# Performance work log

Hardware: AMD Instinct MI355X
Metric: run time of the kernel (lower is better)

Reference implementation:

```python
import jax, jax.numpy as jnp
import numpy as np

B, Q, C, H, N, D, F = 1, 2048, 2048, 1024, 16, 64, 4096
R = Q + C  # relative position encoding length
EPS = 1e-12
NEG = 1e30


def setup_inputs() -> dict:
    key = jax.random.key(0)
    ks = jax.random.split(key, 16)
    s = 0.02
    return dict(
        content_stream=jax.random.normal(ks[0], (B, Q, H), jnp.float32),
        content_mask=jnp.zeros((B, 1, Q, C), jnp.float32),
        context=jax.random.normal(ks[1], (B, C, H), jnp.float32),
        position_encoding=jax.random.normal(ks[2], (B, R, H), jnp.float32),
        content_bias=jax.random.normal(ks[3], (N, D), jnp.float32) * s,
        position_bias=jax.random.normal(ks[4], (N, D), jnp.float32) * s,
        segment_encoding=jax.random.normal(ks[5], (2, N, D), jnp.float32) * s,
        segment_matrix=jax.random.randint(ks[6], (B, Q, C), 0, 2).astype(bool),
        segment_bias=jax.random.normal(ks[7], (N, D), jnp.float32) * s,
        Wq=jax.random.normal(ks[8], (H, N, D), jnp.float32) * s,
        Wk=jax.random.normal(ks[9], (H, N, D), jnp.float32) * s,
        Wv=jax.random.normal(ks[10], (H, N, D), jnp.float32) * s,
        Wr=jax.random.normal(ks[11], (H, N, D), jnp.float32) * s,
        Wo=jax.random.normal(ks[12], (H, N, D), jnp.float32) * s,
        ln1_gamma=jnp.ones((H,), jnp.float32),
        ln1_beta=jnp.zeros((H,), jnp.float32),
        W1=jax.random.normal(ks[13], (H, F), jnp.float32) * s,
        b1=jnp.zeros((F,), jnp.float32),
        W2=jax.random.normal(ks[14], (F, H), jnp.float32) * s,
        b2=jnp.zeros((H,), jnp.float32),
        ln2_gamma=jnp.ones((H,), jnp.float32),
        ln2_beta=jnp.zeros((H,), jnp.float32),
    )


def _layernorm(x, g, b):
    m = jnp.mean(x, axis=-1, keepdims=True)
    v = jnp.mean(jnp.square(x - m), axis=-1, keepdims=True)
    return (x - m) * jax.lax.rsqrt(v + EPS) * g + b


def _rel_shift(x, klen):
    # x: [b, n, q, r] -> shifted [b, n, q, klen] (XLNet reshape trick)
    b, n, q, r = x.shape
    x = x.reshape(b, n, r, q)[:, :, 1:, :].reshape(b, n, q, r - 1)
    return x[:, :, :, :klen]


def reference(content_stream, content_mask, context, position_encoding,
              content_bias, position_bias, segment_encoding, segment_matrix,
              segment_bias, Wq, Wk, Wv, Wr, Wo, ln1_gamma, ln1_beta,
              W1, b1, W2, b2, ln2_gamma, ln2_beta):
    q = jnp.einsum('bqh,hnd->bqnd', content_stream, Wq)
    k = jnp.einsum('bch,hnd->bcnd', context, Wk)
    v = jnp.einsum('bch,hnd->bcnd', context, Wv)
    r = jnp.einsum('brh,hnd->brnd', position_encoding, Wr)

    # content / position / segment bias terms (XLNet relative attention)
    ac = jnp.einsum('bqnd,bcnd->bnqc', q + content_bias, k)
    bd = _rel_shift(jnp.einsum('bqnd,brnd->bnqr', q + position_bias, r),
                    k.shape[1])
    ef = jnp.einsum('bqnd,snd->bnqs', q + segment_bias, segment_encoding)
    ef = jnp.where(segment_matrix[:, None], ef[..., 1:], ef[..., :1])

    scores = (ac + bd + ef) / jnp.sqrt(jnp.float32(D))
    scores = scores - NEG * content_mask  # mask: 1.0 = disallowed
    probs = jax.nn.softmax(scores, axis=-1)

    attn = jnp.einsum('bnqc,bcnd->bqnd', probs, v)
    attn_out = jnp.einsum('bqnd,hnd->bqh', attn, Wo)

    # residual + LN, then FFN, residual + LN (dropout off: training=False)
    ffn_in = _layernorm(attn_out + content_stream, ln1_gamma, ln1_beta)
    ffn_out = jax.nn.relu(ffn_in @ W1 + b1) @ W2 + b2
    return _layernorm(ffn_out + ffn_in, ln2_gamma, ln2_beta)
```

## Files before the change

### kernel.cpp

```cpp
#include <hip/hip_runtime.h>
#include <stdint.h>


typedef unsigned short ushort_t;
typedef __attribute__((ext_vector_type(8))) short bf16x8;
typedef __attribute__((ext_vector_type(4))) float f32x4;

#define QLEN 2048
#define CLEN 2048
#define HDIM 1024
#define NHEAD 16
#define DHEAD 64
#define RLEN 4096
#define FDIM 4096

__device__ __forceinline__ float bf2f(ushort_t u) {
  union { float f; uint32_t i; } x; x.i = ((uint32_t)u) << 16; return x.f;
}
__device__ __forceinline__ ushort_t f2bf(float f) {
  union { float f; uint32_t i; } x; x.f = f;
  uint32_t r = x.i + 0x7fffu + ((x.i >> 16) & 1u);
  return (ushort_t)(r >> 16);
}
__device__ __forceinline__ f32x4 mfma16(bf16x8 a, bf16x8 b, f32x4 c) {
  return __builtin_amdgcn_mfma_f32_16x16x32_bf16(a, b, c, 0, 0, 0);
}
__device__ __forceinline__ bool probe_bf16(const uint32_t* probe) {
  return probe[0] == 0x3F803F80u;
}

typedef const __attribute__((address_space(1))) void* gas_t;
typedef __attribute__((address_space(3))) void* las_t;
__device__ __forceinline__ void glds16(const void* g, void* l) {
  __builtin_amdgcn_global_load_lds((gas_t)(uintptr_t)g, (las_t)(uintptr_t)l, 16, 0, 0);
}

__device__ __forceinline__ void bar_lds() {
  __asm__ volatile("s_waitcnt lgkmcnt(0)\n\ts_barrier" ::: "memory");
}
__device__ __forceinline__ void bar_full() {
  __asm__ volatile("s_waitcnt vmcnt(0) lgkmcnt(0)\n\ts_barrier" ::: "memory");
}

struct ConvJobs {
  const void* src[5];
  const void* mask_src;
  ushort_t* dst[5];
  int n[5];
  int blk0[6];
};

__global__ __launch_bounds__(256) void conv_all(
    ConvJobs J, const uint32_t* __restrict__ probe)
{
  const bool isb = probe_bf16(probe);
  int j = 0;
  #pragma unroll
  for (int t = 1; t < 5; t++) if ((int)blockIdx.x >= J.blk0[t]) j = t;
  const int lb = blockIdx.x - J.blk0[j];
  const int nb = J.blk0[j + 1] - J.blk0[j];
  const int n = J.n[j];
  ushort_t* dst = J.dst[j];
  if (j < 4) {
    const void* src = J.src[j];
    for (int i = lb * 256 + threadIdx.x; i < n; i += nb * 256)
      dst[i] = isb ? ((const ushort_t*)src)[i] : f2bf(((const float*)src)[i]);
  } else {
    const void* sm = J.src[4];
    uint32_t sw = 0;
    #pragma unroll
    for (int t = 0; t < 8; t++) sw |= ((const uint32_t*)sm)[t];
    const bool i8 = sw > 1u;
    for (int i = lb * 256 + threadIdx.x; i < n; i += nb * 256) {
      const int s = i8 ? (int)((const unsigned char*)sm)[i]
                       : (int)((const uint32_t*)sm)[i];
      const float mv = isb ? bf2f(((const ushort_t*)J.mask_src)[i])
                           : ((const float*)J.mask_src)[i];
      const float f = (float)(s ? 1 : 0) + (mv != 0.f ? 2.f : 0.f);
      dst[i] = f2bf(f);
    }
  }
}

struct SmallBatch {
  const void* src[10];
  int n[10];
  int off[10];
};

__global__ __launch_bounds__(256) void convert_small(
    SmallBatch sb, ushort_t* __restrict__ dst, const uint32_t* __restrict__ probe)
{
  const bool isb = probe_bf16(probe);
  const int t = blockIdx.x;
  const void* s = sb.src[t];
  ushort_t* d = dst + sb.off[t];
  for (int i = threadIdx.x; i < sb.n[t]; i += 256)
    d[i] = isb ? ((const ushort_t*)s)[i] : f2bf(((const float*)s)[i]);
}

struct TransJobs { const void* src[4]; ushort_t* dst[4]; };
__global__ __launch_bounds__(256) void transpose4_to_bf16(
    TransJobs T, int R, int C, const uint32_t* __restrict__ probe)
{
  const bool isb = probe_bf16(probe);
  const void* in = T.src[blockIdx.z];
  ushort_t* out = T.dst[blockIdx.z];
  __shared__ ushort_t t[32][33];
  const int bx = blockIdx.x * 32, by = blockIdx.y * 32;
  const int x = threadIdx.x & 31, y0 = threadIdx.x >> 5;
  #pragma unroll
  for (int yy = 0; yy < 32; yy += 8) {
    const size_t idx = (size_t)(by + y0 + yy) * C + bx + x;
    t[y0 + yy][x] = isb ? ((const ushort_t*)in)[idx] : f2bf(((const float*)in)[idx]);
  }
  __syncthreads();
  #pragma unroll
  for (int yy = 0; yy < 32; yy += 8)
    out[(size_t)(bx + y0 + yy) * R + by + x] = t[x][y0 + yy];
}

__global__ __launch_bounds__(256) void transpose_to_bf16(
    const void* __restrict__ in, ushort_t* __restrict__ out, int R, int C,
    const uint32_t* __restrict__ probe)
{
  const bool isb = probe_bf16(probe);
  __shared__ ushort_t t[32][33];
  const int bx = blockIdx.x * 32, by = blockIdx.y * 32;
  const int x = threadIdx.x & 31, y0 = threadIdx.x >> 5;
  #pragma unroll
  for (int yy = 0; yy < 32; yy += 8) {
    const size_t idx = (size_t)(by + y0 + yy) * C + bx + x;
    t[y0 + yy][x] = isb ? ((const ushort_t*)in)[idx] : f2bf(((const float*)in)[idx]);
  }
  __syncthreads();
  #pragma unroll
  for (int yy = 0; yy < 32; yy += 8)
    out[(size_t)(bx + y0 + yy) * R + by + x] = t[x][y0 + yy];
}

__device__ __forceinline__ void gemm_store(
    void* out, const ushort_t* bias, int M, int N, int epi,
    int gm, int gn, float v)
{
  if (epi == 0) {
    ((ushort_t*)out)[(size_t)gm * N + gn] = f2bf(v);
  } else if (epi == 1) {
    ((ushort_t*)out)[(size_t)gn * M + gm] = f2bf(v);
  } else if (epi == 2) {
    ((float*)out)[(size_t)gm * N + gn] = v;
  } else if (epi == 3) {
    v += bf2f(bias[gn]); v = v > 0.f ? v : 0.f;
    ((ushort_t*)out)[(size_t)gm * N + gn] = f2bf(v);
  } else if (epi == 4) {
    v += bf2f(bias[gn]);
    ((float*)out)[(size_t)gm * N + gn] = v;
  } else if (epi == 5) {
    ((ushort_t*)out)[((size_t)(gn >> 6) * M + gm) * 64 + (gn & 63)] = f2bf(v);
  } else {
    if (gn < 1024)
      ((ushort_t*)out)[((size_t)(gn >> 6) * M + gm) * 64 + (gn & 63)] = f2bf(v);
    else
      ((ushort_t*)out)[(size_t)2097152 + (size_t)(gn - 1024) * M + gm] = f2bf(v);
  }
}

__global__ __launch_bounds__(256) void gemm_bt_kernel(
    const ushort_t* __restrict__ A, const ushort_t* __restrict__ Bt,
    const ushort_t* __restrict__ bias, void* __restrict__ out,
    int M, int N, int K, int epi)
{
  __shared__ __attribute__((aligned(16))) ushort_t As[2][128 * 32];
  __shared__ __attribute__((aligned(16))) ushort_t Bs[2][64 * 32];
  const int tid = threadIdx.x;
  const int lane = tid & 63, wave = tid >> 6;
  const int l15 = lane & 15, quad = lane >> 4;
  const int m0 = blockIdx.y * 128, n0 = blockIdx.x * 64;

  const int arow = tid >> 2;
  const int acol = (tid & 3) * 8;

  f32x4 acc[2][4];
  #pragma unroll
  for (int i = 0; i < 2; i++)
    #pragma unroll
    for (int j = 0; j < 4; j++) acc[i][j] = (f32x4){0.f, 0.f, 0.f, 0.f};

  const int KI = K >> 5;
  glds16(&A[(size_t)(m0 + arow) * K + acol], &As[0][tid * 8]);
  glds16(&A[(size_t)(m0 + arow + 64) * K + acol], &As[0][tid * 8 + 2048]);
  glds16(&Bt[(size_t)(n0 + arow) * K + acol], &Bs[0][tid * 8]);
  bar_full();

  for (int ki = 0; ki < KI; ki++) {
    const int b = ki & 1;
    if (ki + 1 < KI) {
      const int k1 = (ki + 1) << 5;
      glds16(&A[(size_t)(m0 + arow) * K + k1 + acol], &As[b ^ 1][tid * 8]);
      glds16(&A[(size_t)(m0 + arow + 64) * K + k1 + acol], &As[b ^ 1][tid * 8 + 2048]);
      glds16(&Bt[(size_t)(n0 + arow) * K + k1 + acol], &Bs[b ^ 1][tid * 8]);
    }
    bf16x8 af[2], bfr[4];
    #pragma unroll
    for (int i = 0; i < 2; i++)
      af[i] = *(const bf16x8*)&As[b][(wave * 32 + i * 16 + l15) * 32 + quad * 8];
    #pragma unroll
    for (int j = 0; j < 4; j++)
      bfr[j] = *(const bf16x8*)&Bs[b][(j * 16 + l15) * 32 + quad * 8];
    #pragma unroll
    for (int i = 0; i < 2; i++)
      #pragma unroll
      for (int j = 0; j < 4; j++)
        acc[i][j] = mfma16(af[i], bfr[j], acc[i][j]);
    bar_full();
  }

  #pragma unroll
  for (int i = 0; i < 2; i++)
    #pragma unroll
    for (int j = 0; j < 4; j++)
      #pragma unroll
      for (int rg = 0; rg < 4; rg++)
        gemm_store(out, bias, M, N, epi,
                   m0 + wave * 32 + i * 16 + quad * 4 + rg,
                   n0 + j * 16 + l15, acc[i][j][rg]);
}

struct Ptr4 { void* p[4]; };
__global__ __launch_bounds__(256) void gemm128_bt_kernel(
    const ushort_t* __restrict__ A, const ushort_t* __restrict__ Bt,
    const ushort_t* __restrict__ bias, Ptr4 outs,
    int M, int N, int K, int Kc, int epi)
{
  __shared__ __attribute__((aligned(16))) ushort_t As[2][128 * 32];
  __shared__ __attribute__((aligned(16))) ushort_t Bs[2][128 * 32];
  const int tid = threadIdx.x;
  const int lane = tid & 63, wave = tid >> 6;
  const int l15 = lane & 15, quad = lane >> 4;
  const int wm = wave >> 1, wn = wave & 1;
  const int m0 = blockIdx.y * 128, n0 = blockIdx.x * 128;
  const int kb = blockIdx.z * Kc;
  void* out = outs.p[blockIdx.z];

  const int arow = tid >> 2;
  const int acol = (tid & 3) * 8;

  f32x4 acc[4][4];
  #pragma unroll
  for (int i = 0; i < 4; i++)
    #pragma unroll
    for (int j = 0; j < 4; j++) acc[i][j] = (f32x4){0.f, 0.f, 0.f, 0.f};

  const int KI = Kc >> 5;
  glds16(&A[(size_t)(m0 + arow) * K + kb + acol], &As[0][tid * 8]);
  glds16(&A[(size_t)(m0 + arow + 64) * K + kb + acol], &As[0][tid * 8 + 2048]);
  glds16(&Bt[(size_t)(n0 + arow) * K + kb + acol], &Bs[0][tid * 8]);
  glds16(&Bt[(size_t)(n0 + arow + 64) * K + kb + acol], &Bs[0][tid * 8 + 2048]);
  bar_full();

  for (int ki = 0; ki < KI; ki++) {
    const int b = ki & 1;
    if (ki + 1 < KI) {
      const int k1 = kb + ((ki + 1) << 5);
      glds16(&A[(size_t)(m0 + arow) * K + k1 + acol], &As[b ^ 1][tid * 8]);
      glds16(&A[(size_t)(m0 + arow + 64) * K + k1 + acol], &As[b ^ 1][tid * 8 + 2048]);
      glds16(&Bt[(size_t)(n0 + arow) * K + k1 + acol], &Bs[b ^ 1][tid * 8]);
      glds16(&Bt[(size_t)(n0 + arow + 64) * K + k1 + acol], &Bs[b ^ 1][tid * 8 + 2048]);
    }
    bf16x8 af[4], bfr[4];
    #pragma unroll
    for (int i = 0; i < 4; i++)
      af[i] = *(const bf16x8*)&As[b][(wm * 64 + i * 16 + l15) * 32 + quad * 8];
    #pragma unroll
    for (int j = 0; j < 4; j++)
      bfr[j] = *(const bf16x8*)&Bs[b][(wn * 64 + j * 16 + l15) * 32 + quad * 8];
    #pragma unroll
    for (int i = 0; i < 4; i++)
      #pragma unroll
      for (int j = 0; j < 4; j++)
        acc[i][j] = mfma16(af[i], bfr[j], acc[i][j]);
    bar_full();
  }

  #pragma unroll
  for (int i = 0; i < 4; i++)
    #pragma unroll
    for (int j = 0; j < 4; j++)
      #pragma unroll
      for (int rg = 0; rg < 4; rg++)
        gemm_store(out, bias, M, N, epi,
                   m0 + wm * 64 + i * 16 + quad * 4 + rg,
                   n0 + wn * 64 + j * 16 + l15, acc[i][j][rg]);
}

__global__ __launch_bounds__(256) void gemm64_bt_kernel(
    const ushort_t* __restrict__ A, const ushort_t* __restrict__ Bt,
    const ushort_t* __restrict__ bias, void* __restrict__ out,
    int M, int N, int K, int epi)
{
  __shared__ __attribute__((aligned(16))) ushort_t As[2][64 * 32];
  __shared__ __attribute__((aligned(16))) ushort_t Bs[2][64 * 32];
  const int tid = threadIdx.x;
  const int lane = tid & 63, wave = tid >> 6;
  const int l15 = lane & 15, quad = lane >> 4;
  const int wm = wave >> 1, wn = wave & 1;
  const int m0 = blockIdx.y * 64, n0 = blockIdx.x * 64;

  const int arow = tid >> 2;
  const int acol = (tid & 3) * 8;

  f32x4 acc[2][2];
  #pragma unroll
  for (int i = 0; i < 2; i++)
    #pragma unroll
    for (int j = 0; j < 2; j++) acc[i][j] = (f32x4){0.f, 0.f, 0.f, 0.f};

  const int KI = K >> 5;
  glds16(&A[(size_t)(m0 + arow) * K + acol], &As[0][tid * 8]);
  glds16(&Bt[(size_t)(n0 + arow) * K + acol], &Bs[0][tid * 8]);
  bar_full();

  for (int ki = 0; ki < KI; ki++) {
    const int b = ki & 1;
    if (ki + 1 < KI) {
      const int k1 = (ki + 1) << 5;
      glds16(&A[(size_t)(m0 + arow) * K + k1 + acol], &As[b ^ 1][tid * 8]);
      glds16(&Bt[(size_t)(n0 + arow) * K + k1 + acol], &Bs[b ^ 1][tid * 8]);
    }
    bf16x8 af[2], bfr[2];
    #pragma unroll
    for (int i = 0; i < 2; i++)
      af[i] = *(const bf16x8*)&As[b][(wm * 32 + i * 16 + l15) * 32 + quad * 8];
    #pragma unroll
    for (int j = 0; j < 2; j++)
      bfr[j] = *(const bf16x8*)&Bs[b][(wn * 32 + j * 16 + l15) * 32 + quad * 8];
    #pragma unroll
    for (int i = 0; i < 2; i++)
      #pragma unroll
      for (int j = 0; j < 2; j++)
        acc[i][j] = mfma16(af[i], bfr[j], acc[i][j]);
    bar_full();
  }

  #pragma unroll
  for (int i = 0; i < 2; i++)
    #pragma unroll
    for (int j = 0; j < 2; j++)
      #pragma unroll
      for (int rg = 0; rg < 4; rg++)
        gemm_store(out, bias, M, N, epi,
                   m0 + wm * 32 + i * 16 + quad * 4 + rg,
                   n0 + wn * 32 + j * 16 + l15, acc[i][j][rg]);
}

#define ESTR 36
#define PSTR2 72
__global__ __launch_bounds__(512, 4) void attn_flash(
    const ushort_t* __restrict__ qh, const ushort_t* __restrict__ kh,
    const ushort_t* __restrict__ vT, const ushort_t* __restrict__ rh,
    const ushort_t* __restrict__ cbias, const ushort_t* __restrict__ pbias,
    const ushort_t* __restrict__ sbias, const ushort_t* __restrict__ senc,
    const ushort_t* __restrict__ fmb, ushort_t* __restrict__ attn)
{
  __shared__ __attribute__((aligned(16))) ushort_t kbuf[2][64 * 64];
  __shared__ __attribute__((aligned(16))) ushort_t vbuf[2][64 * 64];
  __shared__ __attribute__((aligned(16))) ushort_t rbuf[2][96 * 64];
  __shared__ __attribute__((aligned(16))) ushort_t Pbuf[32 * PSTR2];
  __shared__ __attribute__((aligned(16))) float escr[8 * 16 * ESTR];
  __shared__ float wsum[2][4][16];
  __shared__ float e0s[32], e1s[32];

  const int n = blockIdx.x;
  const int q0 = blockIdx.y * 32;
  const int tid = threadIdx.x;
  const int lane = tid & 63, wave = tid >> 6;
  const int l15 = lane & 15, quad = lane >> 4;
  const int hq = wave >> 2, ct = wave & 3;

  const ushort_t* qn = qh + (size_t)n * QLEN * 64;
  const ushort_t* kn = kh + (size_t)n * CLEN * 64;
  const ushort_t* rn = rh + (size_t)n * RLEN * 64;
  const ushort_t* vn = vT + (size_t)n * 64 * CLEN;

  const int srow = lane >> 3;
  const int sg = (lane & 7) ^ srow;

  ushort_t* qpcS = (ushort_t*)escr;
  ushort_t* qppS = qpcS + 32 * 64;
  for (int idx = tid; idx < 32 * 64; idx += 512) {
    const int row = idx >> 6, col = idx & 63;
    const float qv = bf2f(qn[(size_t)(q0 + row) * 64 + col]);
    qpcS[idx] = f2bf(qv + bf2f(cbias[n * DHEAD + col]));
    qppS[idx] = f2bf(qv + bf2f(pbias[n * DHEAD + col]));
  }
  if (wave == 7) {
    const int row = lane & 31, sidx = lane >> 5;
    float a = 0.f;
    for (int d = 0; d < DHEAD; d++)
      a += (bf2f(qn[(size_t)(q0 + row) * 64 + d]) + bf2f(sbias[n * DHEAD + d]))
           * bf2f(senc[(size_t)(sidx * NHEAD + n) * DHEAD + d]);
    if (sidx == 0) e0s[row] = a; else e1s[row] = a;
  }
  __syncthreads();

  const bf16x8* qpc8 = (const bf16x8*)qpcS;
  const bf16x8* qpp8 = (const bf16x8*)qppS;
  bf16x8 qcf[2], qpf[2];
  #pragma unroll
  for (int h = 0; h < 2; h++) {
    qcf[h] = qpc8[(hq * 16 + l15) * 8 + h * 4 + quad];
    qpf[h] = qpp8[(hq * 16 + l15) * 8 + h * 4 + quad];
  }

  {
    const int c0 = 0, ua = c0 - q0 + (QLEN - 32);
    if (wave < 2) {
      const int r0 = wave * 32;
      #pragma unroll
      for (int i = 0; i < 4; i++)
        glds16(kn + (size_t)(c0 + r0 + i * 8 + srow) * 64 + sg * 8, &kbuf[0][(r0 + i * 8) * 64]);
    } else if (wave < 4) {
      const int r0 = (wave - 2) * 32;
      #pragma unroll
      for (int i = 0; i < 4; i++)
        glds16(vn + (size_t)(r0 + i * 8 + srow) * CLEN + c0 + sg * 8, &vbuf[0][(r0 + i * 8) * 64]);
    } else {
      const int r0 = (wave - 4) * 24;
      #pragma unroll
      for (int i = 0; i < 3; i++)
        glds16(rn + (size_t)(ua + r0 + i * 8 + srow) * 64 + sg * 8, &rbuf[0][(r0 + i * 8) * 64]);
    }
  }
  bar_full();

  const float e0v = e0s[hq * 16 + l15], e1v = e1s[hq * 16 + l15];
  const float a0q = e0v * 0.125f;
  const float adq = (e1v - e0v) * 0.125f;

  float* escr_w = escr + wave * (16 * ESTR);
  const int gk0 = quad ^ (l15 & 7);
  const int gk1 = (quad + 4) ^ (l15 & 7);

  float l_row = 0.f;
  f32x4 O = (f32x4){0.f, 0.f, 0.f, 0.f};

  const size_t eoff = (size_t)(q0 + hq * 16 + l15) * CLEN + ct * 16 + quad * 4;

  for (int ci = 0; ci < CLEN / 64; ci++) {
    const int b = ci & 1;

    const uint2 fmv = *(const uint2*)&fmb[eoff + (size_t)ci * 64];

    if (ci + 1 < CLEN / 64) {
      const int c1 = (ci + 1) * 64, ua1 = c1 - q0 + (QLEN - 32);
      if (wave < 2) {
        const int r0 = wave * 32;
        #pragma unroll
        for (int i = 0; i < 4; i++)
          glds16(kn + (size_t)(c1 + r0 + i * 8 + srow) * 64 + sg * 8, &kbuf[b ^ 1][(r0 + i * 8) * 64]);
      } else if (wave < 4) {
        const int r0 = (wave - 2) * 32;
        #pragma unroll
        for (int i = 0; i < 4; i++)
          glds16(vn + (size_t)(r0 + i * 8 + srow) * CLEN + c1 + sg * 8, &vbuf[b ^ 1][(r0 + i * 8) * 64]);
      } else {
        const int r0 = (wave - 4) * 24;
        #pragma unroll
        for (int i = 0; i < 3; i++)
          glds16(rn + (size_t)(ua1 + r0 + i * 8 + srow) * 64 + sg * 8, &rbuf[b ^ 1][(r0 + i * 8) * 64]);
      }
    }

    #pragma unroll
    for (int t = 0; t < 2; t++) {
      const int rrow = ct * 16 + ((1 - hq) + t) * 16 + l15;
      f32x4 e = (f32x4){0.f, 0.f, 0.f, 0.f};
      e = mfma16(*(const bf16x8*)&rbuf[b][rrow * 64 + gk0 * 8], qpf[0], e);
      e = mfma16(*(const bf16x8*)&rbuf[b][rrow * 64 + gk1 * 8], qpf[1], e);
      *(f32x4*)&escr_w[l15 * ESTR + t * 16 + quad * 4] = e;
    }

    const int krow = ct * 16 + l15;
    f32x4 a = (f32x4){0.f, 0.f, 0.f, 0.f};
    a = mfma16(*(const bf16x8*)&kbuf[b][krow * 64 + gk0 * 8], qcf[0], a);
    a = mfma16(*(const bf16x8*)&kbuf[b][krow * 64 + gk1 * 8], qcf[1], a);

    const ushort_t fm4[4] = {(ushort_t)(fmv.x & 0xffff), (ushort_t)(fmv.x >> 16),
                             (ushort_t)(fmv.y & 0xffff), (ushort_t)(fmv.y >> 16)};
    const float* dg = &escr_w[l15 * ESTR + quad * 4 - l15 + 16];
    float p[4], psum = 0.f;
    #pragma unroll
    for (int rg = 0; rg < 4; rg++) {
      const float f = bf2f(fm4[rg]);
      const float mk = floorf(f * 0.5f);
      const float sm = f - 2.f * mk;
      float v = fmaf(a[rg] + dg[rg], 0.125f, fmaf(sm, adq, a0q));
      v = fmaf(mk, -1.0e30f, v);
      p[rg] = __expf(v);
      psum += p[rg];
    }
    psum += __shfl_xor(psum, 16);
    psum += __shfl_xor(psum, 32);
    l_row += psum;

    {
      uint2 pk;
      pk.x = (uint32_t)f2bf(p[0]) | ((uint32_t)f2bf(p[1]) << 16);
      pk.y = (uint32_t)f2bf(p[2]) | ((uint32_t)f2bf(p[3]) << 16);
      *(uint2*)&Pbuf[(hq * 16 + l15) * PSTR2 + ct * 16 + quad * 4] = pk;
    }
    bar_lds();

    const int vrow = ct * 16 + l15;
    const bf16x8 vf0 = *(const bf16x8*)&vbuf[b][vrow * 64 + gk0 * 8];
    const bf16x8 vf1 = *(const bf16x8*)&vbuf[b][vrow * 64 + gk1 * 8];
    const bf16x8 pa0 = *(const bf16x8*)&Pbuf[(hq * 16 + l15) * PSTR2 + quad * 8];
    const bf16x8 pa1 = *(const bf16x8*)&Pbuf[(hq * 16 + l15) * PSTR2 + 32 + quad * 8];
    O = mfma16(pa0, vf0, O);
    O = mfma16(pa1, vf1, O);

    bar_full();
  }

  if (quad == 0) wsum[hq][ct][l15] = l_row;
  __syncthreads();
  const float l = wsum[hq][0][l15] + wsum[hq][1][l15] + wsum[hq][2][l15] + wsum[hq][3][l15];
  const float linv = 1.0f / l;
  float linv4[4];
  #pragma unroll
  for (int rg = 0; rg < 4; rg++) linv4[rg] = __shfl(linv, quad * 4 + rg);
  #pragma unroll
  for (int rg = 0; rg < 4; rg++)
    attn[(size_t)(q0 + hq * 16 + quad * 4 + rg) * HDIM + n * 64 + ct * 16 + l15] =
        f2bf(O[rg] * linv4[rg]);
}

__global__ __launch_bounds__(256) void ln_kernel(
    const float* __restrict__ x0, const float* __restrict__ x1,
    const float* __restrict__ x2, const float* __restrict__ x3,
    const ushort_t* __restrict__ res_bf, const float* __restrict__ res_f,
    const ushort_t* __restrict__ badd,
    const ushort_t* __restrict__ gamma, const ushort_t* __restrict__ beta,
    ushort_t* __restrict__ out_bf, float* __restrict__ out_f,
    void* __restrict__ out_dyn, const uint32_t* __restrict__ probe)
{
  const int row = blockIdx.x, tid = threadIdx.x;
  const int lane = tid & 63, wave = tid >> 6;
  __shared__ float red[8];
  const size_t base = (size_t)row * HDIM;
  float v[4];
  #pragma unroll
  for (int i = 0; i < 4; i++) {
    const int h = tid + i * 256;
    float xv = x0[base + h];
    if (x1) xv += x1[base + h] + x2[base + h] + x3[base + h];
    if (badd) xv += bf2f(badd[h]);
    const float rv = res_bf ? bf2f(res_bf[base + h]) : res_f[base + h];
    v[i] = xv + rv;
  }
  float s = v[0] + v[1] + v[2] + v[3];
  float ss = v[0] * v[0] + v[1] * v[1] + v[2] * v[2] + v[3] * v[3];
  #pragma unroll
  for (int off = 32; off > 0; off >>= 1) {
    s += __shfl_xor(s, off);
    ss += __shfl_xor(ss, off);
  }
  if (lane == 0) { red[wave] = s; red[4 + wave] = ss; }
  __syncthreads();
  s = red[0] + red[1] + red[2] + red[3];
  ss = red[4] + red[5] + red[6] + red[7];
  const float mean = s * (1.0f / HDIM);
  float var = ss * (1.0f / HDIM) - mean * mean;
  var = var > 0.f ? var : 0.f;
  const float rs = rsqrtf(var + 1e-12f);
  const bool outb = out_dyn ? probe_bf16(probe) : false;
  #pragma unroll
  for (int i = 0; i < 4; i++) {
    const int h = tid + i * 256;
    const float y = (v[i] - mean) * rs * bf2f(gamma[h]) + bf2f(beta[h]);
    if (out_bf) out_bf[base + h] = f2bf(y);
    if (out_f)  out_f[base + h] = y;
    if (out_dyn) {
      if (outb) ((ushort_t*)out_dyn)[base + h] = f2bf(y);
      else      ((float*)out_dyn)[base + h] = y;
    }
  }
}

extern "C" void kernel_launch(void* const* d_in, const int* in_sizes, int n_in,
                              void* d_out, int out_size, void* d_ws, size_t ws_size,
                              hipStream_t stream)
{
  (void)in_sizes; (void)n_in; (void)out_size; (void)ws_size;

  const void* cs_r   = d_in[0];
  const void* mask_r = d_in[1];
  const void* ctx_r  = d_in[2];
  const void* pe_r   = d_in[3];
  const void* cb_r   = d_in[4];
  const void* pb_r   = d_in[5];
  const void* senc_r = d_in[6];
  const void* smat   = d_in[7];
  const void* sb_r   = d_in[8];
  const void* Wq_r   = d_in[9];
  const void* Wk_r   = d_in[10];
  const void* Wv_r   = d_in[11];
  const void* Wr_r   = d_in[12];
  const void* Wo_r   = d_in[13];
  const void* g1_r   = d_in[14];
  const void* be1_r  = d_in[15];
  const void* W1_r   = d_in[16];
  const void* b1_r   = d_in[17];
  const void* W2_r   = d_in[18];
  const void* b2_r   = d_in[19];
  const void* g2_r   = d_in[20];
  const void* be2_r  = d_in[21];

  const uint32_t* probe = (const uint32_t*)g1_r;

  char* w = (char*)d_ws;
  #define WSOFF(mb) ((void*)(w + ((size_t)(mb) << 20)))
  ushort_t* fm_b     = (ushort_t*)WSOFF(0);
  ushort_t* Wqt      = (ushort_t*)WSOFF(8);
  ushort_t* Wkt      = (ushort_t*)WSOFF(10);
  ushort_t* Wvt      = (ushort_t*)WSOFF(12);
  ushort_t* Wrt      = (ushort_t*)WSOFF(14);
  ushort_t* W1t      = (ushort_t*)WSOFF(16);
  ushort_t* W2t      = (ushort_t*)WSOFF(24);
  ushort_t* Wo_b     = (ushort_t*)WSOFF(32);
  ushort_t* smalls   = (ushort_t*)WSOFF(34);
  ushort_t* cs_b     = (ushort_t*)WSOFF(35);
  ushort_t* ctx_b    = (ushort_t*)WSOFF(47);
  ushort_t* pe_b     = (ushort_t*)WSOFF(51);
  ushort_t* qbuf     = (ushort_t*)WSOFF(59);
  ushort_t* kbuf     = (ushort_t*)WSOFF(63);
  ushort_t* vTbuf    = (ushort_t*)WSOFF(67);
  ushort_t* rbuf     = (ushort_t*)WSOFF(71);
  ushort_t* attnbuf  = (ushort_t*)WSOFF(79);
  float*    attn_out = (float*)WSOFF(83);
  ushort_t* ffn_in_b = (ushort_t*)WSOFF(91);
  ushort_t* hidden   = (ushort_t*)WSOFF(39);
  float*    ffn_in_f = (float*)WSOFF(71);
  float*    fp0      = (float*)WSOFF(0);
  float*    fp1      = (float*)WSOFF(8);
  float*    fp2      = (float*)WSOFF(59);
  float*    fp3      = (float*)WSOFF(83);

  ushort_t* cb   = smalls + 0;
  ushort_t* pb   = smalls + 1024;
  ushort_t* sb   = smalls + 2048;
  ushort_t* senc = smalls + 3072;
  ushort_t* b1   = smalls + 5120;
  ushort_t* b2   = smalls + 9216;
  ushort_t* g1   = smalls + 10240;
  ushort_t* be1  = smalls + 11264;
  ushort_t* g2   = smalls + 12288;
  ushort_t* be2  = smalls + 13312;

  const dim3 blk(256);

  SmallBatch sbatch;
  const void* ssrc[10] = {cb_r, pb_r, sb_r, senc_r, b1_r, b2_r, g1_r, be1_r, g2_r, be2_r};
  const int   sn[10]   = {1024, 1024, 1024, 2048, 4096, 1024, 1024, 1024, 1024, 1024};
  const int   soff[10] = {0, 1024, 2048, 3072, 5120, 9216, 10240, 11264, 12288, 13312};
  for (int i = 0; i < 10; i++) { sbatch.src[i] = ssrc[i]; sbatch.n[i] = sn[i]; sbatch.off[i] = soff[i]; }
  convert_small<<<10, blk, 0, stream>>>(sbatch, smalls, probe);

  ConvJobs cj;
  cj.src[0] = cs_r;  cj.dst[0] = cs_b;  cj.n[0] = QLEN * HDIM;
  cj.src[1] = ctx_r; cj.dst[1] = ctx_b; cj.n[1] = CLEN * HDIM;
  cj.src[2] = pe_r;  cj.dst[2] = pe_b;  cj.n[2] = RLEN * HDIM;
  cj.src[3] = Wo_r;  cj.dst[3] = Wo_b;  cj.n[3] = HDIM * HDIM;
  cj.src[4] = smat;  cj.dst[4] = fm_b;  cj.n[4] = QLEN * CLEN;
  cj.mask_src = mask_r;
  int pfx = 0;
  for (int i = 0; i < 5; i++) {
    cj.blk0[i] = pfx;
    pfx += (cj.n[i] + 2047) / 2048;
  }
  cj.blk0[5] = pfx;
  conv_all<<<pfx, blk, 0, stream>>>(cj, probe);

  TransJobs tj;
  tj.src[0] = Wq_r; tj.dst[0] = Wqt;
  tj.src[1] = Wk_r; tj.dst[1] = Wkt;
  tj.src[2] = Wv_r; tj.dst[2] = Wvt;
  tj.src[3] = Wr_r; tj.dst[3] = Wrt;
  transpose4_to_bf16<<<dim3(32, 32, 4), blk, 0, stream>>>(tj, HDIM, HDIM, probe);
  transpose_to_bf16<<<dim3(128, 32), blk, 0, stream>>>(W1_r, W1t, HDIM, FDIM, probe);
  transpose_to_bf16<<<dim3(32, 128), blk, 0, stream>>>(W2_r, W2t, FDIM, HDIM, probe);

  gemm64_bt_kernel<<<dim3(16, 32), blk, 0, stream>>>(cs_b,  Wqt, nullptr, qbuf,  QLEN, HDIM, HDIM, 5);
  gemm_bt_kernel<<<dim3(32, 16), blk, 0, stream>>>(ctx_b, Wkt, nullptr, kbuf, CLEN, 2048, HDIM, 6);
  gemm_bt_kernel<<<dim3(16, 32), blk, 0, stream>>>(pe_b,  Wrt, nullptr, rbuf,  RLEN, HDIM, HDIM, 5);

  attn_flash<<<dim3(NHEAD, QLEN / 32), dim3(512), 0, stream>>>(
      qbuf, kbuf, vTbuf, rbuf, cb, pb, sb, senc, fm_b, attnbuf);

  gemm64_bt_kernel<<<dim3(16, 32), blk, 0, stream>>>(attnbuf, Wo_b, nullptr, attn_out, QLEN, HDIM, HDIM, 2);

  ln_kernel<<<QLEN, blk, 0, stream>>>(attn_out, nullptr, nullptr, nullptr,
                                      cs_b, nullptr, nullptr, g1, be1,
                                      ffn_in_b, ffn_in_f, nullptr, probe);

  Ptr4 o1; o1.p[0] = hidden; o1.p[1] = o1.p[2] = o1.p[3] = nullptr;
  gemm128_bt_kernel<<<dim3(32, 16, 1), blk, 0, stream>>>(
      ffn_in_b, W1t, b1, o1, QLEN, FDIM, HDIM, HDIM, 3);

  Ptr4 o2; o2.p[0] = fp0; o2.p[1] = fp1; o2.p[2] = fp2; o2.p[3] = fp3;
  gemm128_bt_kernel<<<dim3(8, 16, 4), blk, 0, stream>>>(
      hidden, W2t, nullptr, o2, QLEN, HDIM, FDIM, FDIM / 4, 2);

  ln_kernel<<<QLEN, blk, 0, stream>>>(fp0, fp1, fp2, fp3,
                                      nullptr, ffn_in_f, b2, g2, be2,
                                      nullptr, nullptr, d_out, probe);
  #undef WSOFF
}
```

Baseline: 475.4 us.

## Merge Q/K/V/R projections into one grouped GEMM launch and unroll attention loop

The three separate projection GEMM launches (Q, fused K+V, R) become one grouped 128x128-tile kernel whose blocks pick their sub-problem from a prefix table. This cuts launch overhead and fills the device better with larger tiles. The flash-attention main loop is unrolled by two with precomputed staging pointers, so address math inside the loop is reduced. The score path also uses a packed bf16 convert instruction and simpler mask unpacking. The larger tiles use more registers and LDS per block, which may lower occupancy.

```diff
diff --git a/kernel.cpp b/kernel.cpp
--- a/kernel.cpp
+++ b/kernel.cpp
@@ -21,6 +21,9 @@
   union { float f; uint32_t i; } x; x.f = f;
   uint32_t r = x.i + 0x7fffu + ((x.i >> 16) & 1u);
   return (ushort_t)(r >> 16);
+}
+__device__ __forceinline__ float u2f(uint32_t u) {
+  union { float f; uint32_t i; } x; x.i = u; return x.f;
 }
 __device__ __forceinline__ f32x4 mfma16(bf16x8 a, bf16x8 b, f32x4 c) {
   return __builtin_amdgcn_mfma_f32_16x16x32_bf16(a, b, c, 0, 0, 0);
@@ -165,67 +168,6 @@
   }
 }
 
-__global__ __launch_bounds__(256) void gemm_bt_kernel(
-    const ushort_t* __restrict__ A, const ushort_t* __restrict__ Bt,
-    const ushort_t* __restrict__ bias, void* __restrict__ out,
-    int M, int N, int K, int epi)
-{
-  __shared__ __attribute__((aligned(16))) ushort_t As[2][128 * 32];
-  __shared__ __attribute__((aligned(16))) ushort_t Bs[2][64 * 32];
-  const int tid = threadIdx.x;
-  const int lane = tid & 63, wave = tid >> 6;
-  const int l15 = lane & 15, quad = lane >> 4;
-  const int m0 = blockIdx.y * 128, n0 = blockIdx.x * 64;
-
-  const int arow = tid >> 2;
-  const int acol = (tid & 3) * 8;
-
-  f32x4 acc[2][4];
-  #pragma unroll
-  for (int i = 0; i < 2; i++)
-    #pragma unroll
-    for (int j = 0; j < 4; j++) acc[i][j] = (f32x4){0.f, 0.f, 0.f, 0.f};
-
-  const int KI = K >> 5;
-  glds16(&A[(size_t)(m0 + arow) * K + acol], &As[0][tid * 8]);
-  glds16(&A[(size_t)(m0 + arow + 64) * K + acol], &As[0][tid * 8 + 2048]);
-  glds16(&Bt[(size_t)(n0 + arow) * K + acol], &Bs[0][tid * 8]);
-  bar_full();
-
-  for (int ki = 0; ki < KI; ki++) {
-    const int b = ki & 1;
-    if (ki + 1 < KI) {
-      const int k1 = (ki + 1) << 5;
-      glds16(&A[(size_t)(m0 + arow) * K + k1 + acol], &As[b ^ 1][tid * 8]);
-      glds16(&A[(size_t)(m0 + arow + 64) * K + k1 + acol], &As[b ^ 1][tid * 8 + 2048]);
-      glds16(&Bt[(size_t)(n0 + arow) * K + k1 + acol], &Bs[b ^ 1][tid * 8]);
-    }
-    bf16x8 af[2], bfr[4];
-    #pragma unroll
-    for (int i = 0; i < 2; i++)
-      af[i] = *(const bf16x8*)&As[b][(wave * 32 + i * 16 + l15) * 32 + quad * 8];
-    #pragma unroll
-    for (int j = 0; j < 4; j++)
-      bfr[j] = *(const bf16x8*)&Bs[b][(j * 16 + l15) * 32 + quad * 8];
-    #pragma unroll
-    for (int i = 0; i < 2; i++)
-      #pragma unroll
-      for (int j = 0; j < 4; j++)
-        acc[i][j] = mfma16(af[i], bfr[j], acc[i][j]);
-    bar_full();
-  }
-
-  #pragma unroll
-  for (int i = 0; i < 2; i++)
-    #pragma unroll
-    for (int j = 0; j < 4; j++)
-      #pragma unroll
-      for (int rg = 0; rg < 4; rg++)
-        gemm_store(out, bias, M, N, epi,
-                   m0 + wave * 32 + i * 16 + quad * 4 + rg,
-                   n0 + j * 16 + l15, acc[i][j][rg]);
-}
-
 struct Ptr4 { void* p[4]; };
 __global__ __launch_bounds__(256) void gemm128_bt_kernel(
     const ushort_t* __restrict__ A, const ushort_t* __restrict__ Bt,
@@ -293,6 +235,83 @@
                    n0 + wn * 64 + j * 16 + l15, acc[i][j][rg]);
 }
 
+struct MultiG {
+  const ushort_t* A[3]; const ushort_t* Bt[3]; void* out[3];
+  int M[3], N[3], epi[3], bxsh[3], blk0[4];
+};
+
+__global__ __launch_bounds__(256) void gemm128_multi_kernel(MultiG G, int K)
+{
+  int j = 0;
+  #pragma unroll
+  for (int t = 1; t < 3; t++) if ((int)blockIdx.x >= G.blk0[t]) j = t;
+  const int lb = blockIdx.x - G.blk0[j];
+  const int bx = lb & ((1 << G.bxsh[j]) - 1);
+  const int by = lb >> G.bxsh[j];
+  const ushort_t* __restrict__ A = G.A[j];
+  const ushort_t* __restrict__ Bt = G.Bt[j];
+  void* out = G.out[j];
+  const int M = G.M[j], N = G.N[j], epi = G.epi[j];
+
+  __shared__ __attribute__((aligned(16))) ushort_t As[2][128 * 32];
+  __shared__ __attribute__((aligned(16))) ushort_t Bs[2][128 * 32];
+  const int tid = threadIdx.x;
+  const int lane = tid & 63, wave = tid >> 6;
+  const int l15 = lane & 15, quad = lane >> 4;
+  const int wm = wave >> 1, wn = wave & 1;
+  const int m0 = by * 128, n0 = bx * 128;
+
+  const int arow = tid >> 2;
+  const int acol = (tid & 3) * 8;
+
+  f32x4 acc[4][4];
+  #pragma unroll
+  for (int i = 0; i < 4; i++)
+    #pragma unroll
+    for (int jj = 0; jj < 4; jj++) acc[i][jj] = (f32x4){0.f, 0.f, 0.f, 0.f};
+
+  const int KI = K >> 5;
+  glds16(&A[(size_t)(m0 + arow) * K + acol], &As[0][tid * 8]);
+  glds16(&A[(size_t)(m0 + arow + 64) * K + acol], &As[0][tid * 8 + 2048]);
+  glds16(&Bt[(size_t)(n0 + arow) * K + acol], &Bs[0][tid * 8]);
+  glds16(&Bt[(size_t)(n0 + arow + 64) * K + acol], &Bs[0][tid * 8 + 2048]);
+  bar_full();
+
+  for (int ki = 0; ki < KI; ki++) {
+    const int b = ki & 1;
+    if (ki + 1 < KI) {
+      const int k1 = (ki + 1) << 5;
+      glds16(&A[(size_t)(m0 + arow) * K + k1 + acol], &As[b ^ 1][tid * 8]);
+      glds16(&A[(size_t)(m0 + arow + 64) * K + k1 + acol], &As[b ^ 1][tid * 8 + 2048]);
+      glds16(&Bt[(size_t)(n0 + arow) * K + k1 + acol], &Bs[b ^ 1][tid * 8]);
+      glds16(&Bt[(size_t)(n0 + arow + 64) * K + k1 + acol], &Bs[b ^ 1][tid * 8 + 2048]);
+    }
+    bf16x8 af[4], bfr[4];
+    #pragma unroll
+    for (int i = 0; i < 4; i++)
+      af[i] = *(const bf16x8*)&As[b][(wm * 64 + i * 16 + l15) * 32 + quad * 8];
+    #pragma unroll
+    for (int jj = 0; jj < 4; jj++)
+      bfr[jj] = *(const bf16x8*)&Bs[b][(wn * 64 + jj * 16 + l15) * 32 + quad * 8];
+    #pragma unroll
+    for (int i = 0; i < 4; i++)
+      #pragma unroll
+      for (int jj = 0; jj < 4; jj++)
+        acc[i][jj] = mfma16(af[i], bfr[jj], acc[i][jj]);
+    bar_full();
+  }
+
+  #pragma unroll
+  for (int i = 0; i < 4; i++)
+    #pragma unroll
+    for (int jj = 0; jj < 4; jj++)
+      #pragma unroll
+      for (int rg = 0; rg < 4; rg++)
+        gemm_store(out, nullptr, M, N, epi,
+                   m0 + wm * 64 + i * 16 + quad * 4 + rg,
+                   n0 + wn * 64 + jj * 16 + l15, acc[i][jj][rg]);
+}
+
 __global__ __launch_bounds__(256) void gemm64_bt_kernel(
     const ushort_t* __restrict__ A, const ushort_t* __restrict__ Bt,
     const ushort_t* __restrict__ bias, void* __restrict__ out,
@@ -405,32 +424,40 @@
 
   const bf16x8* qpc8 = (const bf16x8*)qpcS;
   const bf16x8* qpp8 = (const bf16x8*)qppS;
-  bf16x8 qcf[2], qpf[2];
-  #pragma unroll
-  for (int h = 0; h < 2; h++) {
-    qcf[h] = qpc8[(hq * 16 + l15) * 8 + h * 4 + quad];
-    qpf[h] = qpp8[(hq * 16 + l15) * 8 + h * 4 + quad];
-  }
-
-  {
-    const int c0 = 0, ua = c0 - q0 + (QLEN - 32);
-    if (wave < 2) {
-      const int r0 = wave * 32;
-      #pragma unroll
-      for (int i = 0; i < 4; i++)
-        glds16(kn + (size_t)(c0 + r0 + i * 8 + srow) * 64 + sg * 8, &kbuf[0][(r0 + i * 8) * 64]);
-    } else if (wave < 4) {
-      const int r0 = (wave - 2) * 32;
-      #pragma unroll
-      for (int i = 0; i < 4; i++)
-        glds16(vn + (size_t)(r0 + i * 8 + srow) * CLEN + c0 + sg * 8, &vbuf[0][(r0 + i * 8) * 64]);
-    } else {
-      const int r0 = (wave - 4) * 24;
-      #pragma unroll
-      for (int i = 0; i < 3; i++)
-        glds16(rn + (size_t)(ua + r0 + i * 8 + srow) * 64 + sg * 8, &rbuf[0][(r0 + i * 8) * 64]);
-    }
-  }
+  const bf16x8 qcf0 = qpc8[(hq * 16 + l15) * 8 + quad];
+  const bf16x8 qcf1 = qpc8[(hq * 16 + l15) * 8 + 4 + quad];
+  const bf16x8 qpf0 = qpp8[(hq * 16 + l15) * 8 + quad];
+  const bf16x8 qpf1 = qpp8[(hq * 16 + l15) * 8 + 4 + quad];
+
+  const ushort_t* gsrc;
+  size_t sstride, sadv;
+  bool s4;
+  ushort_t *d0, *d1;
+  if (wave < 2) {
+    const int r0 = wave * 32;
+    gsrc = kn + (size_t)(r0 + srow) * 64 + sg * 8;
+    sstride = 512; sadv = 4096; s4 = true;
+    d0 = &kbuf[0][r0 * 64]; d1 = &kbuf[1][r0 * 64];
+  } else if (wave < 4) {
+    const int r0 = (wave - 2) * 32;
+    gsrc = vn + (size_t)(r0 + srow) * CLEN + sg * 8;
+    sstride = (size_t)8 * CLEN; sadv = 64; s4 = true;
+    d0 = &vbuf[0][r0 * 64]; d1 = &vbuf[1][r0 * 64];
+  } else {
+    const int r0 = (wave - 4) * 24;
+    gsrc = rn + (size_t)(QLEN - 32 - q0 + r0 + srow) * 64 + sg * 8;
+    sstride = 512; sadv = 4096; s4 = false;
+    d0 = &rbuf[0][r0 * 64]; d1 = &rbuf[1][r0 * 64];
+  }
+
+  #define STAGE(D) do { \
+    glds16(gsrc, (D)); \
+    glds16(gsrc + sstride, (D) + 512); \
+    glds16(gsrc + 2 * sstride, (D) + 1024); \
+    if (s4) glds16(gsrc + 3 * sstride, (D) + 1536); \
+    gsrc += sadv; } while (0)
+
+  STAGE(d0);
   bar_full();
 
   const float e0v = e0s[hq * 16 + l15], e1v = e1s[hq * 16 + l15];
@@ -444,83 +471,66 @@
   float l_row = 0.f;
   f32x4 O = (f32x4){0.f, 0.f, 0.f, 0.f};
 
-  const size_t eoff = (size_t)(q0 + hq * 16 + l15) * CLEN + ct * 16 + quad * 4;
-
-  for (int ci = 0; ci < CLEN / 64; ci++) {
-    const int b = ci & 1;
-
-    const uint2 fmv = *(const uint2*)&fmb[eoff + (size_t)ci * 64];
-
-    if (ci + 1 < CLEN / 64) {
-      const int c1 = (ci + 1) * 64, ua1 = c1 - q0 + (QLEN - 32);
-      if (wave < 2) {
-        const int r0 = wave * 32;
-        #pragma unroll
-        for (int i = 0; i < 4; i++)
-          glds16(kn + (size_t)(c1 + r0 + i * 8 + srow) * 64 + sg * 8, &kbuf[b ^ 1][(r0 + i * 8) * 64]);
-      } else if (wave < 4) {
-        const int r0 = (wave - 2) * 32;
-        #pragma unroll
-        for (int i = 0; i < 4; i++)
-          glds16(vn + (size_t)(r0 + i * 8 + srow) * CLEN + c1 + sg * 8, &vbuf[b ^ 1][(r0 + i * 8) * 64]);
-      } else {
-        const int r0 = (wave - 4) * 24;
-        #pragma unroll
-        for (int i = 0; i < 3; i++)
-          glds16(rn + (size_t)(ua1 + r0 + i * 8 + srow) * 64 + sg * 8, &rbuf[b ^ 1][(r0 + i * 8) * 64]);
-      }
-    }
-
-    #pragma unroll
-    for (int t = 0; t < 2; t++) {
-      const int rrow = ct * 16 + ((1 - hq) + t) * 16 + l15;
-      f32x4 e = (f32x4){0.f, 0.f, 0.f, 0.f};
-      e = mfma16(*(const bf16x8*)&rbuf[b][rrow * 64 + gk0 * 8], qpf[0], e);
-      e = mfma16(*(const bf16x8*)&rbuf[b][rrow * 64 + gk1 * 8], qpf[1], e);
-      *(f32x4*)&escr_w[l15 * ESTR + t * 16 + quad * 4] = e;
-    }
-
-    const int krow = ct * 16 + l15;
-    f32x4 a = (f32x4){0.f, 0.f, 0.f, 0.f};
-    a = mfma16(*(const bf16x8*)&kbuf[b][krow * 64 + gk0 * 8], qcf[0], a);
-    a = mfma16(*(const bf16x8*)&kbuf[b][krow * 64 + gk1 * 8], qcf[1], a);
-
-    const ushort_t fm4[4] = {(ushort_t)(fmv.x & 0xffff), (ushort_t)(fmv.x >> 16),
-                             (ushort_t)(fmv.y & 0xffff), (ushort_t)(fmv.y >> 16)};
-    const float* dg = &escr_w[l15 * ESTR + quad * 4 - l15 + 16];
-    float p[4], psum = 0.f;
-    #pragma unroll
-    for (int rg = 0; rg < 4; rg++) {
-      const float f = bf2f(fm4[rg]);
-      const float mk = floorf(f * 0.5f);
-      const float sm = f - 2.f * mk;
-      float v = fmaf(a[rg] + dg[rg], 0.125f, fmaf(sm, adq, a0q));
-      v = fmaf(mk, -1.0e30f, v);
-      p[rg] = __expf(v);
-      psum += p[rg];
-    }
-    psum += __shfl_xor(psum, 16);
-    psum += __shfl_xor(psum, 32);
-    l_row += psum;
-
-    {
-      uint2 pk;
-      pk.x = (uint32_t)f2bf(p[0]) | ((uint32_t)f2bf(p[1]) << 16);
-      pk.y = (uint32_t)f2bf(p[2]) | ((uint32_t)f2bf(p[3]) << 16);
-      *(uint2*)&Pbuf[(hq * 16 + l15) * PSTR2 + ct * 16 + quad * 4] = pk;
-    }
-    bar_lds();
-
-    const int vrow = ct * 16 + l15;
-    const bf16x8 vf0 = *(const bf16x8*)&vbuf[b][vrow * 64 + gk0 * 8];
-    const bf16x8 vf1 = *(const bf16x8*)&vbuf[b][vrow * 64 + gk1 * 8];
-    const bf16x8 pa0 = *(const bf16x8*)&Pbuf[(hq * 16 + l15) * PSTR2 + quad * 8];
-    const bf16x8 pa1 = *(const bf16x8*)&Pbuf[(hq * 16 + l15) * PSTR2 + 32 + quad * 8];
-    O = mfma16(pa0, vf0, O);
-    O = mfma16(pa1, vf1, O);
-
-    bar_full();
-  }
+  const ushort_t* fmp = fmb + (size_t)(q0 + hq * 16 + l15) * CLEN + ct * 16 + quad * 4;
+
+  #define DO_CHUNK(kb, rb, vb, FMV) do { \
+    _Pragma("unroll") \
+    for (int t = 0; t < 2; t++) { \
+      const int rrow = ct * 16 + ((1 - hq) + t) * 16 + l15; \
+      f32x4 e = (f32x4){0.f, 0.f, 0.f, 0.f}; \
+      e = mfma16(*(const bf16x8*)&(rb)[rrow * 64 + gk0 * 8], qpf0, e); \
+      e = mfma16(*(const bf16x8*)&(rb)[rrow * 64 + gk1 * 8], qpf1, e); \
+      *(f32x4*)&escr_w[l15 * ESTR + t * 16 + quad * 4] = e; \
+    } \
+    const int krow = ct * 16 + l15; \
+    f32x4 a = (f32x4){0.f, 0.f, 0.f, 0.f}; \
+    a = mfma16(*(const bf16x8*)&(kb)[krow * 64 + gk0 * 8], qcf0, a); \
+    a = mfma16(*(const bf16x8*)&(kb)[krow * 64 + gk1 * 8], qcf1, a); \
+    float fv4[4]; \
+    fv4[0] = u2f(FMV.x << 16); fv4[1] = u2f(FMV.x & 0xFFFF0000u); \
+    fv4[2] = u2f(FMV.y << 16); fv4[3] = u2f(FMV.y & 0xFFFF0000u); \
+    const float* dg = &escr_w[l15 * ESTR + quad * 4 - l15 + 16]; \
+    float p[4], psum = 0.f; \
+    _Pragma("unroll") \
+    for (int rg = 0; rg < 4; rg++) { \
+      const float f = fv4[rg]; \
+      const float mk = floorf(f * 0.5f); \
+      const float sm = f - 2.f * mk; \
+      float v = fmaf(a[rg] + dg[rg], 0.125f, fmaf(sm, adq, a0q)); \
+      v = fmaf(mk, -1.0e30f, v); \
+      p[rg] = __expf(v); \
+      psum += p[rg]; \
+    } \
+    psum += __shfl_xor(psum, 16); \
+    psum += __shfl_xor(psum, 32); \
+    l_row += psum; \
+    { uint32_t pk0, pk1; \
+      asm("v_cvt_pk_bf16_f32 %0, %1, %2" : "=v"(pk0) : "v"(p[0]), "v"(p[1])); \
+      asm("v_cvt_pk_bf16_f32 %0, %1, %2" : "=v"(pk1) : "v"(p[2]), "v"(p[3])); \
+      uint2 pkk; pkk.x = pk0; pkk.y = pk1; \
+      *(uint2*)&Pbuf[(hq * 16 + l15) * PSTR2 + ct * 16 + quad * 4] = pkk; } \
+    bar_lds(); \
+    { const int vrow = ct * 16 + l15; \
+      const bf16x8 vf0 = *(const bf16x8*)&(vb)[vrow * 64 + gk0 * 8]; \
+      const bf16x8 vf1 = *(const bf16x8*)&(vb)[vrow * 64 + gk1 * 8]; \
+      const bf16x8 pa0 = *(const bf16x8*)&Pbuf[(hq * 16 + l15) * PSTR2 + quad * 8]; \
+      const bf16x8 pa1 = *(const bf16x8*)&Pbuf[(hq * 16 + l15) * PSTR2 + 32 + quad * 8]; \
+      O = mfma16(pa0, vf0, O); \
+      O = mfma16(pa1, vf1, O); } \
+    bar_full(); \
+  } while (0)
+
+  for (int ci = 0; ci < CLEN / 64; ci += 2) {
+    const uint2 fmva = *(const uint2*)fmp;
+    const uint2 fmvb = *(const uint2*)(fmp + 64);
+    fmp += 128;
+    STAGE(d1);
+    DO_CHUNK(kbuf[0], rbuf[0], vbuf[0], fmva);
+    if (ci + 2 < CLEN / 64) STAGE(d0);
+    DO_CHUNK(kbuf[1], rbuf[1], vbuf[1], fmvb);
+  }
+  #undef DO_CHUNK
+  #undef STAGE
 
   if (quad == 0) wsum[hq][ct][l15] = l_row;
   __syncthreads();
@@ -690,9 +700,12 @@
   transpose_to_bf16<<<dim3(128, 32), blk, 0, stream>>>(W1_r, W1t, HDIM, FDIM, probe);
   transpose_to_bf16<<<dim3(32, 128), blk, 0, stream>>>(W2_r, W2t, FDIM, HDIM, probe);
 
-  gemm64_bt_kernel<<<dim3(16, 32), blk, 0, stream>>>(cs_b,  Wqt, nullptr, qbuf,  QLEN, HDIM, HDIM, 5);
-  gemm_bt_kernel<<<dim3(32, 16), blk, 0, stream>>>(ctx_b, Wkt, nullptr, kbuf, CLEN, 2048, HDIM, 6);
-  gemm_bt_kernel<<<dim3(16, 32), blk, 0, stream>>>(pe_b,  Wrt, nullptr, rbuf,  RLEN, HDIM, HDIM, 5);
+  MultiG mg;
+  mg.A[0] = cs_b;  mg.Bt[0] = Wqt; mg.out[0] = qbuf; mg.M[0] = QLEN; mg.N[0] = HDIM; mg.epi[0] = 5; mg.bxsh[0] = 3;
+  mg.A[1] = ctx_b; mg.Bt[1] = Wkt; mg.out[1] = kbuf; mg.M[1] = CLEN; mg.N[1] = 2048; mg.epi[1] = 6; mg.bxsh[1] = 4;
+  mg.A[2] = pe_b;  mg.Bt[2] = Wrt; mg.out[2] = rbuf; mg.M[2] = RLEN; mg.N[2] = HDIM; mg.epi[2] = 5; mg.bxsh[2] = 3;
+  mg.blk0[0] = 0; mg.blk0[1] = 128; mg.blk0[2] = 384; mg.blk0[3] = 640;
+  gemm128_multi_kernel<<<dim3(640), blk, 0, stream>>>(mg, HDIM);
 
   attn_flash<<<dim3(NHEAD, QLEN / 32), dim3(512), 0, stream>>>(
       qbuf, kbuf, vTbuf, rbuf, cb, pb, sb, senc, fm_b, attnbuf);
```

New measurement: 459.7 us. 1.03x faster.
